# Optimization experiments

Hardware: AMD Instinct MI355X
Metric: run time of the kernel (lower is better)

The kernel has to match this reference:

```python
import jax, jax.numpy as jnp
import numpy as np

N = 100000
E = 1600000
IN_CH = 128
HID = 16
HEADS = 4
OUT_CH = 2
EDGE_DIM = 3
NEG_SLOPE = 0.2


def gat_layer(x, src, dst, e_feat, W, att_src, att_dst, We, att_edge, bias, H, C, concat):
    # x: [N, Fin] -> projected [N, H, C]
    xs = (x @ W).reshape(-1, H, C)
    a_src = jnp.sum(xs * att_src, axis=-1)          # [N, H]
    a_dst = jnp.sum(xs * att_dst, axis=-1)          # [N, H]
    ee = (e_feat @ We).reshape(-1, H, C)            # [E, H, C]
    a_edge = jnp.sum(ee * att_edge, axis=-1)        # [E, H]
    alpha = a_src[src] + a_dst[dst] + a_edge        # [E, H]
    alpha = jax.nn.leaky_relu(alpha, NEG_SLOPE)
    # segment softmax over incoming edges of each dst node
    seg_max = jax.ops.segment_max(alpha, dst, num_segments=N)
    alpha = jnp.exp(alpha - seg_max[dst])
    seg_sum = jax.ops.segment_sum(alpha, dst, num_segments=N)
    alpha = alpha / (seg_sum[dst] + 1e-16)
    # weighted message aggregation
    msg = xs[src] * alpha[:, :, None]               # [E, H, C]
    out = jax.ops.segment_sum(msg, dst, num_segments=N)  # [N, H, C]
    out = out.reshape(-1, H * C) if concat else out.mean(axis=1)
    return out + bias


def setup_inputs() -> dict:
    key = jax.random.key(0)
    ks = jax.random.split(key, 24)
    g = lambda i, shape, scale=0.1: jax.random.normal(ks[i], shape, dtype=jnp.float32) * scale
    inp = {
        "x": jax.random.normal(ks[0], (N, IN_CH), dtype=jnp.float32),
        "edge_index": jax.random.randint(ks[1], (2, E), 0, N, dtype=jnp.int32),
        "edge_feat": jax.random.normal(ks[2], (E, EDGE_DIM), dtype=jnp.float32),
        # edge MLP
        "Em1": g(3, (EDGE_DIM, EDGE_DIM)), "eb1": g(4, (EDGE_DIM,)),
        "Em2": g(5, (EDGE_DIM, EDGE_DIM)), "eb2": g(6, (EDGE_DIM,)),
        # conv1: in -> HID per head, HEADS heads, concat
        "W1": g(7, (IN_CH, HEADS * HID)),
        "as1": g(8, (HEADS, HID)), "ad1": g(9, (HEADS, HID)),
        "We1": g(10, (EDGE_DIM, HEADS * HID)), "ae1": g(11, (HEADS, HID)),
        "b1": g(12, (HEADS * HID,)),
        # conv2: HEADS*HID -> OUT_CH, 1 head, no concat
        "W2": g(13, (HEADS * HID, OUT_CH)),
        "as2": g(14, (1, OUT_CH)), "ad2": g(15, (1, OUT_CH)),
        "We2": g(16, (EDGE_DIM, OUT_CH)), "ae2": g(17, (1, OUT_CH)),
        "b2": g(18, (OUT_CH,)),
    }
    return inp


def reference(x, edge_index, edge_feat,
              Em1, eb1, Em2, eb2,
              W1, as1, ad1, We1, ae1, b1,
              W2, as2, ad2, We2, ae2, b2):
    src, dst = edge_index[0], edge_index[1]
    # edge MLP: Linear -> ReLU -> Linear
    e = jax.nn.relu(edge_feat @ Em1 + eb1) @ Em2 + eb2
    # dropout layers are identity in eval mode
    h = gat_layer(x, src, dst, e, W1, as1, ad1, We1, ae1, b1, HEADS, HID, concat=True)
    h = jax.nn.elu(h)
    out = gat_layer(h, src, dst, e, W2, as2, ad2, We2, ae2, b2, 1, OUT_CH, concat=False)
    return out
```

## Files before the change

### kernel.cpp

```cpp
#include <hip/hip_runtime.h>
#include <hip/hip_fp16.h>
#include <math.h>
#include <stdint.h>

#define NEG_SLOPE 0.2f
#define SCAN_TILE 2048

__device__ __forceinline__ float leaky(float a) { return a > 0.f ? a : NEG_SLOPE * a; }
__device__ __forceinline__ __half2 u2h2(unsigned u) { return *reinterpret_cast<__half2*>(&u); }

__global__ __launch_bounds__(256) void k_pw(const int* __restrict__ dst, int* __restrict__ deg8,
                                            int* __restrict__ pw, int E, int N,
                                            const float* __restrict__ We1, const float* __restrict__ ae1,
                                            const float* __restrict__ We2, const float* __restrict__ ae2,
                                            float* __restrict__ cw) {
    if (blockIdx.x == 0 && threadIdx.x == 0) {
        for (int i = 0; i < 3; i++)
            for (int h = 0; h < 4; h++) {
                float s = 0.f;
                for (int m = 0; m < 16; m++) s += We1[i*64 + h*16 + m] * ae1[h*16 + m];
                cw[i*4 + h] = s;
            }
        for (int i = 0; i < 3; i++) cw[12 + i] = We2[i*2]*ae2[0] + We2[i*2+1]*ae2[1];
    }
    int c = blockIdx.x & 7;
    int* deg = deg8 + (size_t)c * N;
    unsigned ctag = (unsigned)c << 28;
    int base = (blockIdx.x * blockDim.x + threadIdx.x) * 4;
    if (base >= E) return;
    if (base + 3 < E) {
        int4 dv = *reinterpret_cast<const int4*>(&dst[base]);
        int4 pv;
        pv.x = atomicAdd(&deg[dv.x], 1) | ctag;
        pv.y = atomicAdd(&deg[dv.y], 1) | ctag;
        pv.z = atomicAdd(&deg[dv.z], 1) | ctag;
        pv.w = atomicAdd(&deg[dv.w], 1) | ctag;
        *reinterpret_cast<int4*>(&pw[base]) = pv;
    } else {
        for (int i = base; i < E; i++) pw[i] = atomicAdd(&deg[dst[i]], 1) | ctag;
    }
}

__global__ __launch_bounds__(256) void k_scan_partial(const int* __restrict__ deg8, int* __restrict__ tsum, int N) {
    __shared__ int sh[256];
    int b = blockIdx.x, t = threadIdx.x;
    int base = b * SCAN_TILE + t * 8;
    int s = 0;
    if (base + 8 <= N) {
        for (int c = 0; c < 8; c++) {
            const int4* p4 = reinterpret_cast<const int4*>(deg8 + (size_t)c * N + base);
            int4 a = p4[0], bb = p4[1];
            s += a.x + a.y + a.z + a.w + bb.x + bb.y + bb.z + bb.w;
        }
    } else if (base < N) {
        for (int i = base; i < N; i++)
            for (int c = 0; c < 8; c++) s += deg8[(size_t)c * N + i];
    }
    sh[t] = s; __syncthreads();
    for (int o = 128; o > 0; o >>= 1) { if (t < o) sh[t] += sh[t + o]; __syncthreads(); }
    if (t == 0) tsum[b] = sh[0];
}

__global__ void k_scan_tsum(const int* __restrict__ tsum, int* __restrict__ toff,
                            int* __restrict__ rowptr, int nb, int N) {
    if (threadIdx.x == 0 && blockIdx.x == 0) {
        int run = 0;
        for (int i = 0; i < nb; i++) { toff[i] = run; run += tsum[i]; }
        rowptr[N] = run;
    }
}

__global__ __launch_bounds__(256) void k_scan_final(const int* __restrict__ deg8, const int* __restrict__ toff,
        int* __restrict__ rowptr, uint4* __restrict__ slotrec, int N) {
    __shared__ int sh[256];
    int b = blockIdx.x, t = threadIdx.x;
    int base = b * SCAN_TILE + t * 8;
    int vt[8]; int s = 0;
    #pragma unroll
    for (int i = 0; i < 8; i++) {
        int idx = base + i; int tot = 0;
        if (idx < N) {
            #pragma unroll
            for (int c = 0; c < 8; c++) tot += deg8[(size_t)c * N + idx];
        }
        vt[i] = tot; s += tot;
    }
    sh[t] = s; __syncthreads();
    for (int o = 1; o < 256; o <<= 1) {
        int u = (t >= o) ? sh[t - o] : 0;
        __syncthreads();
        sh[t] += u;
        __syncthreads();
    }
    int run = sh[t] - s + toff[b];
    #pragma unroll
    for (int i = 0; i < 8; i++) {
        int idx = base + i;
        if (idx < N) {
            rowptr[idx] = run;
            unsigned lo = 0, hi = 0; int off = 0;
            #pragma unroll
            for (int c = 0; c < 8; c++) {
                unsigned v = (unsigned)off & 0xFFu;
                if (c < 4) lo |= v << (8*c); else hi |= v << (8*(c-4));
                off += deg8[(size_t)c * N + idx];
            }
            slotrec[idx] = make_uint4((unsigned)run, lo, hi, 0u);
            run += vt[i];
        }
    }
}

__global__ __launch_bounds__(256) void k_proj1(const float* __restrict__ x, const float* __restrict__ W1,
        const float* __restrict__ as1, const float* __restrict__ ad1,
        __half* __restrict__ xs1h, float* __restrict__ as1v, float* __restrict__ ad1v, int N) {
    __shared__ float xr[32][128];
    int tid = threadIdx.x;
    int wave = tid >> 6, lane = tid & 63;
    int nbase = blockIdx.x * 32;
    if (nbase + 32 <= N) {
        const float4* x4 = reinterpret_cast<const float4*>(x + (size_t)nbase * 128);
        #pragma unroll
        for (int i = 0; i < 4; i++) {
            int idx = tid + i * 256;
            reinterpret_cast<float4*>(&xr[0][0])[idx] = x4[idx];
        }
    } else {
        for (int i = 0; i < 16; i++) {
            int flat = tid + i * 256;
            int row = flat >> 7, col = flat & 127;
            int n = nbase + row; if (n >= N) n = N - 1;
            xr[row][col] = x[(size_t)n * 128 + col];
        }
    }
    __syncthreads();
    int cc = lane & 15, kk = lane >> 4;
    int nw = wave * 8;
    const float4* W4 = reinterpret_cast<const float4*>(W1);
    float4 acc[8];
    #pragma unroll
    for (int m = 0; m < 8; m++) acc[m] = make_float4(0.f, 0.f, 0.f, 0.f);
    #pragma unroll 4
    for (int k = kk; k < 128; k += 4) {
        float4 wv = W4[k * 16 + cc];
        #pragma unroll
        for (int m = 0; m < 8; m++) {
            float xv = xr[nw + m][k];
            acc[m].x = fmaf(xv, wv.x, acc[m].x);
            acc[m].y = fmaf(xv, wv.y, acc[m].y);
            acc[m].z = fmaf(xv, wv.z, acc[m].z);
            acc[m].w = fmaf(xv, wv.w, acc[m].w);
        }
    }
    float a_s0 = as1[4*cc], a_s1 = as1[4*cc+1], a_s2 = as1[4*cc+2], a_s3 = as1[4*cc+3];
    float a_d0 = ad1[4*cc], a_d1 = ad1[4*cc+1], a_d2 = ad1[4*cc+2], a_d3 = ad1[4*cc+3];
    #pragma unroll
    for (int m = 0; m < 8; m++) {
        float4 a = acc[m];
        a.x += __shfl_xor(a.x, 16, 64); a.y += __shfl_xor(a.y, 16, 64);
        a.z += __shfl_xor(a.z, 16, 64); a.w += __shfl_xor(a.w, 16, 64);
        a.x += __shfl_xor(a.x, 32, 64); a.y += __shfl_xor(a.y, 32, 64);
        a.z += __shfl_xor(a.z, 32, 64); a.w += __shfl_xor(a.w, 32, 64);
        float ps = a.x*a_s0 + a.y*a_s1 + a.z*a_s2 + a.w*a_s3;
        float pd = a.x*a_d0 + a.y*a_d1 + a.z*a_d2 + a.w*a_d3;
        ps += __shfl_xor(ps, 1, 64); ps += __shfl_xor(ps, 2, 64);
        pd += __shfl_xor(pd, 1, 64); pd += __shfl_xor(pd, 2, 64);
        if (kk == 0) {
            int n = nbase + nw + m; if (n >= N) n = N - 1;
            __half2 h01 = __halves2half2(__float2half_rn(a.x), __float2half_rn(a.y));
            __half2 h23 = __halves2half2(__float2half_rn(a.z), __float2half_rn(a.w));
            uint2 st;
            st.x = *reinterpret_cast<unsigned*>(&h01);
            st.y = *reinterpret_cast<unsigned*>(&h23);
            *reinterpret_cast<uint2*>(&xs1h[(size_t)n*64 + 4*cc]) = st;
            if ((cc & 3) == 0) {
                int h = cc >> 2;
                as1v[n*4 + h] = ps;
                ad1v[n*4 + h] = pd;
            }
        }
    }
}

__global__ __launch_bounds__(256) void k_payload(const float* __restrict__ ef,
                       const float* __restrict__ Em1, const float* __restrict__ eb1,
                       const float* __restrict__ Em2, const float* __restrict__ eb2,
                       const float* __restrict__ cw,
                       const int* __restrict__ src, const int* __restrict__ dst,
                       const int* __restrict__ pw,
                       const float4* __restrict__ as1v4,
                       const uint4* __restrict__ slotrec,
                       uint4* __restrict__ csr_pk, int E) {
    int base = (blockIdx.x * blockDim.x + threadIdx.x) * 4;
    if (base >= E) return;
    int cnt = min(4, E - base);

    float f[4][3]; int sv[4], dv[4], pv[4];
    if (cnt == 4) {
        const float4* ef4 = reinterpret_cast<const float4*>(ef);
        float4 a = ef4[base*3/4 + 0], b = ef4[base*3/4 + 1], c = ef4[base*3/4 + 2];
        f[0][0]=a.x; f[0][1]=a.y; f[0][2]=a.z;
        f[1][0]=a.w; f[1][1]=b.x; f[1][2]=b.y;
        f[2][0]=b.z; f[2][1]=b.w; f[2][2]=c.x;
        f[3][0]=c.y; f[3][1]=c.z; f[3][2]=c.w;
        int4 s4 = *reinterpret_cast<const int4*>(&src[base]);
        int4 d4 = *reinterpret_cast<const int4*>(&dst[base]);
        int4 p4 = *reinterpret_cast<const int4*>(&pw[base]);
        sv[0]=s4.x; sv[1]=s4.y; sv[2]=s4.z; sv[3]=s4.w;
        dv[0]=d4.x; dv[1]=d4.y; dv[2]=d4.z; dv[3]=d4.w;
        pv[0]=p4.x; pv[1]=p4.y; pv[2]=p4.z; pv[3]=p4.w;
    } else {
        for (int i = 0; i < cnt; i++) {
            f[i][0]=ef[(base+i)*3+0]; f[i][1]=ef[(base+i)*3+1]; f[i][2]=ef[(base+i)*3+2];
            sv[i]=src[base+i]; dv[i]=dst[base+i]; pv[i]=pw[base+i];
        }
    }

    #pragma unroll
    for (int i = 0; i < 4; i++) {
        if (i >= cnt) break;
        float f0=f[i][0], f1=f[i][1], f2=f[i][2];
        float t0 = fmaxf(f0*Em1[0]+f1*Em1[3]+f2*Em1[6]+eb1[0], 0.f);
        float t1 = fmaxf(f0*Em1[1]+f1*Em1[4]+f2*Em1[7]+eb1[1], 0.f);
        float t2 = fmaxf(f0*Em1[2]+f1*Em1[5]+f2*Em1[8]+eb1[2], 0.f);
        float u0 = t0*Em2[0]+t1*Em2[3]+t2*Em2[6]+eb2[0];
        float u1 = t0*Em2[1]+t1*Em2[4]+t2*Em2[7]+eb2[1];
        float u2 = t0*Em2[2]+t1*Em2[5]+t2*Em2[8]+eb2[2];
        int s = sv[i], d = dv[i];
        float4 av = as1v4[s];
        uint4  r  = slotrec[d];
        int c  = ((unsigned)pv[i]) >> 28;
        int ps = pv[i] & 0x0FFFFFFF;
        unsigned pre = ((c < 4) ? (r.y >> (8*c)) : (r.z >> (8*(c-4)))) & 0xFFu;
        int slot = (int)r.x + (int)pre + ps;
        float b0 = av.x + u0*cw[0] + u1*cw[4] + u2*cw[8];
        float b1 = av.y + u0*cw[1] + u1*cw[5] + u2*cw[9];
        float b2 = av.z + u0*cw[2] + u1*cw[6] + u2*cw[10];
        float b3 = av.w + u0*cw[3] + u1*cw[7] + u2*cw[11];
        float e2 = u0*cw[12] + u1*cw[13] + u2*cw[14];
        __half2 lo = __halves2half2(__float2half_rn(b0), __float2half_rn(b1));
        __half2 hi = __halves2half2(__float2half_rn(b2), __float2half_rn(b3));
        uint4 pki;
        pki.x = (unsigned)s;
        pki.y = *reinterpret_cast<unsigned*>(&lo);
        pki.z = *reinterpret_cast<unsigned*>(&hi);
        pki.w = *reinterpret_cast<unsigned*>(&e2);
        csr_pk[slot] = pki;
    }
}

__global__ __launch_bounds__(256, 4) void k_gat1(
        const int* __restrict__ rowptr, const uint4* __restrict__ csr_pk,
        const __half* __restrict__ xs1h, const float4* __restrict__ ad1v4,
        const float* __restrict__ b1, const float* __restrict__ W2,
        const float* __restrict__ as2, const float* __restrict__ ad2,
        float2* __restrict__ pk2, float* __restrict__ ad2v, int N) {
    int wave = threadIdx.x >> 6, lane = threadIdx.x & 63;
    int d = blockIdx.x * 4 + wave;
    if (d >= N) return;
    int beg = rowptr[d], end = rowptr[d+1];
    float4 ad4 = ad1v4[d];
    int cg = lane & 15, e4 = lane >> 4;
    int hh = cg >> 2;
    const __half* xbase = xs1h + 4 * cg;
    float4 acc = make_float4(0.f, 0.f, 0.f, 0.f);
    float4 wv  = make_float4(0.f, 0.f, 0.f, 0.f);
    for (int off = beg; off < end; off += 16) {
        int j = off + cg;
        bool valid = j < end;
        uint4 p = valid ? csr_pk[j] : make_uint4(0u, 0u, 0u, 0u);
        int si = (int)p.x;
        float w0 = 0.f, w1 = 0.f, w2 = 0.f, w3 = 0.f;
        if (valid) {
            __half2 l01 = u2h2(p.y), l23 = u2h2(p.z);
            w0 = __expf(leaky(__low2float(l01)  + ad4.x));
            w1 = __expf(leaky(__high2float(l01) + ad4.y));
            w2 = __expf(leaky(__low2float(l23)  + ad4.z));
            w3 = __expf(leaky(__high2float(l23) + ad4.w));
        }
        wv.x += w0; wv.y += w1; wv.z += w2; wv.w += w3;
        __half2 wy2 = __halves2half2(__float2half_rn(w0), __float2half_rn(w1));
        __half2 wz2 = __halves2half2(__float2half_rn(w2), __float2half_rn(w3));
        unsigned wy = *reinterpret_cast<unsigned*>(&wy2);
        unsigned wz = *reinterpret_cast<unsigned*>(&wz2);
        int st0, st1, st2, st3; float wt0, wt1, wt2, wt3;
        {
            int sl0 = 0*4 + e4, sl1 = 1*4 + e4, sl2 = 2*4 + e4, sl3 = 3*4 + e4;
            st0 = __shfl(si, sl0, 16); st1 = __shfl(si, sl1, 16);
            st2 = __shfl(si, sl2, 16); st3 = __shfl(si, sl3, 16);
            unsigned y0 = __shfl(wy, sl0, 16), z0 = __shfl(wz, sl0, 16);
            unsigned y1 = __shfl(wy, sl1, 16), z1 = __shfl(wz, sl1, 16);
            unsigned y2 = __shfl(wy, sl2, 16), z2 = __shfl(wz, sl2, 16);
            unsigned y3 = __shfl(wy, sl3, 16), z3 = __shfl(wz, sl3, 16);
            unsigned q0 = (hh < 2) ? y0 : z0;
            unsigned q1 = (hh < 2) ? y1 : z1;
            unsigned q2 = (hh < 2) ? y2 : z2;
            unsigned q3 = (hh < 2) ? y3 : z3;
            wt0 = (hh & 1) ? __high2float(u2h2(q0)) : __low2float(u2h2(q0));
            wt1 = (hh & 1) ? __high2float(u2h2(q1)) : __low2float(u2h2(q1));
            wt2 = (hh & 1) ? __high2float(u2h2(q2)) : __low2float(u2h2(q2));
            wt3 = (hh & 1) ? __high2float(u2h2(q3)) : __low2float(u2h2(q3));
        }
        uint2 g0 = *reinterpret_cast<const uint2*>(xbase + ((size_t)st0 << 6));
        uint2 g1 = *reinterpret_cast<const uint2*>(xbase + ((size_t)st1 << 6));
        uint2 g2 = *reinterpret_cast<const uint2*>(xbase + ((size_t)st2 << 6));
        uint2 g3 = *reinterpret_cast<const uint2*>(xbase + ((size_t)st3 << 6));
        __half2 a, b;
        a = u2h2(g0.x); b = u2h2(g0.y);
        acc.x = fmaf(wt0, __low2float(a), acc.x); acc.y = fmaf(wt0, __high2float(a), acc.y);
        acc.z = fmaf(wt0, __low2float(b), acc.z); acc.w = fmaf(wt0, __high2float(b), acc.w);
        a = u2h2(g1.x); b = u2h2(g1.y);
        acc.x = fmaf(wt1, __low2float(a), acc.x); acc.y = fmaf(wt1, __high2float(a), acc.y);
        acc.z = fmaf(wt1, __low2float(b), acc.z); acc.w = fmaf(wt1, __high2float(b), acc.w);
        a = u2h2(g2.x); b = u2h2(g2.y);
        acc.x = fmaf(wt2, __low2float(a), acc.x); acc.y = fmaf(wt2, __high2float(a), acc.y);
        acc.z = fmaf(wt2, __low2float(b), acc.z); acc.w = fmaf(wt2, __high2float(b), acc.w);
        a = u2h2(g3.x); b = u2h2(g3.y);
        acc.x = fmaf(wt3, __low2float(a), acc.x); acc.y = fmaf(wt3, __high2float(a), acc.y);
        acc.z = fmaf(wt3, __low2float(b), acc.z); acc.w = fmaf(wt3, __high2float(b), acc.w);
    }
    acc.x += __shfl_xor(acc.x, 16, 64); acc.y += __shfl_xor(acc.y, 16, 64);
    acc.z += __shfl_xor(acc.z, 16, 64); acc.w += __shfl_xor(acc.w, 16, 64);
    acc.x += __shfl_xor(acc.x, 32, 64); acc.y += __shfl_xor(acc.y, 32, 64);
    acc.z += __shfl_xor(acc.z, 32, 64); acc.w += __shfl_xor(acc.w, 32, 64);
    #pragma unroll
    for (int o = 1; o <= 8; o <<= 1) {
        wv.x += __shfl_xor(wv.x, o, 16); wv.y += __shfl_xor(wv.y, o, 16);
        wv.z += __shfl_xor(wv.z, o, 16); wv.w += __shfl_xor(wv.w, o, 16);
    }
    float sm = (hh == 0) ? wv.x : (hh == 1) ? wv.y : (hh == 2) ? wv.z : wv.w;
    float inv = 1.f / (sm + 1e-16f);
    float v0 = acc.x * inv + b1[4*cg + 0];
    float v1 = acc.y * inv + b1[4*cg + 1];
    float v2 = acc.z * inv + b1[4*cg + 2];
    float v3 = acc.w * inv + b1[4*cg + 3];
    v0 = v0 > 0.f ? v0 : expm1f(v0);
    v1 = v1 > 0.f ? v1 : expm1f(v1);
    v2 = v2 > 0.f ? v2 : expm1f(v2);
    v3 = v3 > 0.f ? v3 : expm1f(v3);
    float p0 = v0*W2[(4*cg+0)*2] + v1*W2[(4*cg+1)*2] + v2*W2[(4*cg+2)*2] + v3*W2[(4*cg+3)*2];
    float p1 = v0*W2[(4*cg+0)*2+1] + v1*W2[(4*cg+1)*2+1] + v2*W2[(4*cg+2)*2+1] + v3*W2[(4*cg+3)*2+1];
    #pragma unroll
    for (int o = 1; o <= 8; o <<= 1) { p0 += __shfl_xor(p0, o, 16); p1 += __shfl_xor(p1, o, 16); }
    if (lane == 0) {
        float2 q;
        q.x = p0*as2[0] + p1*as2[1];
        __half2 xv = __halves2half2(__float2half_rn(p0), __float2half_rn(p1));
        q.y = *reinterpret_cast<float*>(&xv);
        pk2[d] = q;
        ad2v[d] = p0*ad2[0] + p1*ad2[1];
    }
}

__global__ __launch_bounds__(256) void k_gat2(
        const int* __restrict__ rowptr, const uint4* __restrict__ csr_pk,
        const float2* __restrict__ pk2, const float* __restrict__ ad2v,
        const float* __restrict__ b2, float* __restrict__ out, int N) {
    int t = blockIdx.x * blockDim.x + threadIdx.x;
    int d = t >> 4, j16 = t & 15;
    if (d >= N) return;
    int beg = rowptr[d], end = rowptr[d+1];
    float add = ad2v[d];
    float sm = 0.f, p0 = 0.f, p1 = 0.f;
    for (int off = beg; off < end; off += 16) {
        int j = off + j16;
        if (j < end) {
            uint4 p = csr_pk[j];
            int s = (int)p.x;
            float ea2 = *reinterpret_cast<float*>(&p.w);
            float2 q = pk2[s];
            float w = __expf(leaky(q.x + add + ea2));
            __half2 xv = *reinterpret_cast<__half2*>(&q.y);
            p0 = fmaf(w, __low2float(xv), p0);
            p1 = fmaf(w, __high2float(xv), p1);
            sm += w;
        }
    }
    #pragma unroll
    for (int o = 1; o < 16; o <<= 1) {
        sm += __shfl_xor(sm, o, 16);
        p0 += __shfl_xor(p0, o, 16);
        p1 += __shfl_xor(p1, o, 16);
    }
    if (j16 == 0) {
        float inv = 1.f / (sm + 1e-16f);
        out[d*2+0] = p0*inv + b2[0];
        out[d*2+1] = p1*inv + b2[1];
    }
}

extern "C" void kernel_launch(void* const* d_in, const int* in_sizes, int n_in,
                              void* d_out, int out_size, void* d_ws, size_t ws_size,
                              hipStream_t stream) {
    const float* x   = (const float*)d_in[0];
    const int*   ei  = (const int*)d_in[1];
    const float* ef  = (const float*)d_in[2];
    const float* Em1 = (const float*)d_in[3];
    const float* eb1 = (const float*)d_in[4];
    const float* Em2 = (const float*)d_in[5];
    const float* eb2 = (const float*)d_in[6];
    const float* W1  = (const float*)d_in[7];
    const float* as1 = (const float*)d_in[8];
    const float* ad1 = (const float*)d_in[9];
    const float* We1 = (const float*)d_in[10];
    const float* ae1 = (const float*)d_in[11];
    const float* b1  = (const float*)d_in[12];
    const float* W2  = (const float*)d_in[13];
    const float* as2 = (const float*)d_in[14];
    const float* ad2 = (const float*)d_in[15];
    const float* We2 = (const float*)d_in[16];
    const float* ae2 = (const float*)d_in[17];
    const float* b2  = (const float*)d_in[18];

    const int N = in_sizes[0] / 128;
    const int E = in_sizes[1] / 2;
    const int* srcp = ei;
    const int* dstp = ei + E;

    uintptr_t w = (uintptr_t)d_ws;
    auto alloc = [&](size_t bytes) -> void* {
        uintptr_t p = w; w += (bytes + 255) & ~(size_t)255; return (void*)p;
    };
    const int nb = (N + SCAN_TILE - 1) / SCAN_TILE;
    int*    deg8    = (int*)alloc((size_t)8 * N * sizeof(int));
    int*    rowptr  = (int*)alloc(((size_t)N + 1) * sizeof(int));
    int*    tsum    = (int*)alloc((size_t)nb * sizeof(int));
    int*    toff    = (int*)alloc((size_t)(nb + 1) * sizeof(int));
    float*  cw      = (float*)alloc(16 * sizeof(float));
    int*    pw      = (int*)alloc((size_t)E * sizeof(int));
    uint4*  slotrec = (uint4*)alloc((size_t)N * sizeof(uint4));
    uint4*  csr_pk  = (uint4*)alloc((size_t)E * sizeof(uint4));
    __half* xs1h    = (__half*)alloc((size_t)N * 64 * sizeof(__half));
    float*  as1v    = (float*)alloc((size_t)N * 4 * sizeof(float));
    float*  ad1v    = (float*)alloc((size_t)N * 4 * sizeof(float));
    float2* pk2     = (float2*)alloc((size_t)N * sizeof(float2));
    float*  ad2v    = (float*)alloc((size_t)N * sizeof(float));

    const int B = 256;

    hipMemsetAsync(deg8, 0, (size_t)8 * N * sizeof(int), stream);
    k_pw<<<(E/4+B-1)/B + 1, B, 0, stream>>>(dstp, deg8, pw, E, N, We1, ae1, We2, ae2, cw);
    k_scan_partial<<<nb, 256, 0, stream>>>(deg8, tsum, N);
    k_scan_tsum<<<1, 64, 0, stream>>>(tsum, toff, rowptr, nb, N);
    k_scan_final<<<nb, 256, 0, stream>>>(deg8, toff, rowptr, slotrec, N);
    k_proj1<<<(N+31)/32, 256, 0, stream>>>(x, W1, as1, ad1, xs1h, as1v, ad1v, N);
    k_payload<<<(E/4+B-1)/B + 1, B, 0, stream>>>(ef, Em1, eb1, Em2, eb2, cw,
                                                 srcp, dstp, pw, (const float4*)as1v,
                                                 slotrec, csr_pk, E);
    k_gat1<<<(N+3)/4, 256, 0, stream>>>(rowptr, csr_pk, xs1h, (const float4*)ad1v,
                                        b1, W2, as2, ad2, pk2, ad2v, N);
    k_gat2<<<(N*16+B-1)/B, B, 0, stream>>>(rowptr, csr_pk, pk2, ad2v, b2, (float*)d_out, N);
}
```

Measured before the change: 254.1 us.

## Remap GAT1 wave lanes to head-major layout to cut exp and shuffle work

Reassigns the 64 lanes in the layer-1 aggregation kernel so each 16-lane group owns one head. Each lane now computes one exp per edge instead of four, and broadcasts float weights directly, dropping the half packing and select logic. The reductions at the end are rewritten to match the new lane map. In exchange, each gather now reads 16 contiguous halves per head rather than spreading one source row across the wave, which may change memory coalescing.

```diff
diff --git a/kernel.cpp b/kernel.cpp
--- a/kernel.cpp
+++ b/kernel.cpp
@@ -260,47 +260,35 @@
     if (d >= N) return;
     int beg = rowptr[d], end = rowptr[d+1];
     float4 ad4 = ad1v4[d];
-    int cg = lane & 15, e4 = lane >> 4;
-    int hh = cg >> 2;
-    const __half* xbase = xs1h + 4 * cg;
+    int sub = lane & 15;
+    int hh  = lane >> 4;
+    int e4  = (lane >> 2) & 3;
+    int cq  = lane & 3;
+    float adh = (hh == 0) ? ad4.x : (hh == 1) ? ad4.y : (hh == 2) ? ad4.z : ad4.w;
+    const __half* xbase = xs1h + (hh * 16 + cq * 4);
     float4 acc = make_float4(0.f, 0.f, 0.f, 0.f);
-    float4 wv  = make_float4(0.f, 0.f, 0.f, 0.f);
+    float wsum = 0.f;
     for (int off = beg; off < end; off += 16) {
-        int j = off + cg;
+        int j = off + sub;
         bool valid = j < end;
         uint4 p = valid ? csr_pk[j] : make_uint4(0u, 0u, 0u, 0u);
         int si = (int)p.x;
-        float w0 = 0.f, w1 = 0.f, w2 = 0.f, w3 = 0.f;
+        float w = 0.f;
         if (valid) {
-            __half2 l01 = u2h2(p.y), l23 = u2h2(p.z);
-            w0 = __expf(leaky(__low2float(l01)  + ad4.x));
-            w1 = __expf(leaky(__high2float(l01) + ad4.y));
-            w2 = __expf(leaky(__low2float(l23)  + ad4.z));
-            w3 = __expf(leaky(__high2float(l23) + ad4.w));
-        }
-        wv.x += w0; wv.y += w1; wv.z += w2; wv.w += w3;
-        __half2 wy2 = __halves2half2(__float2half_rn(w0), __float2half_rn(w1));
-        __half2 wz2 = __halves2half2(__float2half_rn(w2), __float2half_rn(w3));
-        unsigned wy = *reinterpret_cast<unsigned*>(&wy2);
-        unsigned wz = *reinterpret_cast<unsigned*>(&wz2);
-        int st0, st1, st2, st3; float wt0, wt1, wt2, wt3;
-        {
-            int sl0 = 0*4 + e4, sl1 = 1*4 + e4, sl2 = 2*4 + e4, sl3 = 3*4 + e4;
-            st0 = __shfl(si, sl0, 16); st1 = __shfl(si, sl1, 16);
-            st2 = __shfl(si, sl2, 16); st3 = __shfl(si, sl3, 16);
-            unsigned y0 = __shfl(wy, sl0, 16), z0 = __shfl(wz, sl0, 16);
-            unsigned y1 = __shfl(wy, sl1, 16), z1 = __shfl(wz, sl1, 16);
-            unsigned y2 = __shfl(wy, sl2, 16), z2 = __shfl(wz, sl2, 16);
-            unsigned y3 = __shfl(wy, sl3, 16), z3 = __shfl(wz, sl3, 16);
-            unsigned q0 = (hh < 2) ? y0 : z0;
-            unsigned q1 = (hh < 2) ? y1 : z1;
-            unsigned q2 = (hh < 2) ? y2 : z2;
-            unsigned q3 = (hh < 2) ? y3 : z3;
-            wt0 = (hh & 1) ? __high2float(u2h2(q0)) : __low2float(u2h2(q0));
-            wt1 = (hh & 1) ? __high2float(u2h2(q1)) : __low2float(u2h2(q1));
-            wt2 = (hh & 1) ? __high2float(u2h2(q2)) : __low2float(u2h2(q2));
-            wt3 = (hh & 1) ? __high2float(u2h2(q3)) : __low2float(u2h2(q3));
-        }
+            unsigned lw = (hh < 2) ? p.y : p.z;
+            __half2 lh = u2h2(lw);
+            float lg = (hh & 1) ? __high2float(lh) : __low2float(lh);
+            w = __expf(leaky(lg + adh));
+        }
+        wsum += w;
+        int st0 = __shfl(si, e4 + 0, 16);
+        int st1 = __shfl(si, e4 + 4, 16);
+        int st2 = __shfl(si, e4 + 8, 16);
+        int st3 = __shfl(si, e4 + 12, 16);
+        float wt0 = __shfl(w, e4 + 0, 16);
+        float wt1 = __shfl(w, e4 + 4, 16);
+        float wt2 = __shfl(w, e4 + 8, 16);
+        float wt3 = __shfl(w, e4 + 12, 16);
         uint2 g0 = *reinterpret_cast<const uint2*>(xbase + ((size_t)st0 << 6));
         uint2 g1 = *reinterpret_cast<const uint2*>(xbase + ((size_t)st1 << 6));
         uint2 g2 = *reinterpret_cast<const uint2*>(xbase + ((size_t)st2 << 6));
@@ -319,29 +307,33 @@
         acc.x = fmaf(wt3, __low2float(a), acc.x); acc.y = fmaf(wt3, __high2float(a), acc.y);
         acc.z = fmaf(wt3, __low2float(b), acc.z); acc.w = fmaf(wt3, __high2float(b), acc.w);
     }
-    acc.x += __shfl_xor(acc.x, 16, 64); acc.y += __shfl_xor(acc.y, 16, 64);
-    acc.z += __shfl_xor(acc.z, 16, 64); acc.w += __shfl_xor(acc.w, 16, 64);
-    acc.x += __shfl_xor(acc.x, 32, 64); acc.y += __shfl_xor(acc.y, 32, 64);
-    acc.z += __shfl_xor(acc.z, 32, 64); acc.w += __shfl_xor(acc.w, 32, 64);
-    #pragma unroll
-    for (int o = 1; o <= 8; o <<= 1) {
-        wv.x += __shfl_xor(wv.x, o, 16); wv.y += __shfl_xor(wv.y, o, 16);
-        wv.z += __shfl_xor(wv.z, o, 16); wv.w += __shfl_xor(wv.w, o, 16);
-    }
-    float sm = (hh == 0) ? wv.x : (hh == 1) ? wv.y : (hh == 2) ? wv.z : wv.w;
-    float inv = 1.f / (sm + 1e-16f);
-    float v0 = acc.x * inv + b1[4*cg + 0];
-    float v1 = acc.y * inv + b1[4*cg + 1];
-    float v2 = acc.z * inv + b1[4*cg + 2];
-    float v3 = acc.w * inv + b1[4*cg + 3];
-    v0 = v0 > 0.f ? v0 : expm1f(v0);
-    v1 = v1 > 0.f ? v1 : expm1f(v1);
-    v2 = v2 > 0.f ? v2 : expm1f(v2);
-    v3 = v3 > 0.f ? v3 : expm1f(v3);
-    float p0 = v0*W2[(4*cg+0)*2] + v1*W2[(4*cg+1)*2] + v2*W2[(4*cg+2)*2] + v3*W2[(4*cg+3)*2];
-    float p1 = v0*W2[(4*cg+0)*2+1] + v1*W2[(4*cg+1)*2+1] + v2*W2[(4*cg+2)*2+1] + v3*W2[(4*cg+3)*2+1];
-    #pragma unroll
-    for (int o = 1; o <= 8; o <<= 1) { p0 += __shfl_xor(p0, o, 16); p1 += __shfl_xor(p1, o, 16); }
+    acc.x += __shfl_xor(acc.x, 4, 64); acc.y += __shfl_xor(acc.y, 4, 64);
+    acc.z += __shfl_xor(acc.z, 4, 64); acc.w += __shfl_xor(acc.w, 4, 64);
+    acc.x += __shfl_xor(acc.x, 8, 64); acc.y += __shfl_xor(acc.y, 8, 64);
+    acc.z += __shfl_xor(acc.z, 8, 64); acc.w += __shfl_xor(acc.w, 8, 64);
+    wsum += __shfl_xor(wsum, 1, 64);
+    wsum += __shfl_xor(wsum, 2, 64);
+    wsum += __shfl_xor(wsum, 4, 64);
+    wsum += __shfl_xor(wsum, 8, 64);
+    float inv = 1.f / (wsum + 1e-16f);
+    float p0 = 0.f, p1 = 0.f;
+    if (e4 == 0) {
+        int cb = hh * 16 + cq * 4;
+        float v0 = acc.x * inv + b1[cb + 0];
+        float v1 = acc.y * inv + b1[cb + 1];
+        float v2 = acc.z * inv + b1[cb + 2];
+        float v3 = acc.w * inv + b1[cb + 3];
+        v0 = v0 > 0.f ? v0 : expm1f(v0);
+        v1 = v1 > 0.f ? v1 : expm1f(v1);
+        v2 = v2 > 0.f ? v2 : expm1f(v2);
+        v3 = v3 > 0.f ? v3 : expm1f(v3);
+        p0 = v0*W2[(cb+0)*2]   + v1*W2[(cb+1)*2]   + v2*W2[(cb+2)*2]   + v3*W2[(cb+3)*2];
+        p1 = v0*W2[(cb+0)*2+1] + v1*W2[(cb+1)*2+1] + v2*W2[(cb+2)*2+1] + v3*W2[(cb+3)*2+1];
+    }
+    p0 += __shfl_xor(p0, 1, 64);  p1 += __shfl_xor(p1, 1, 64);
+    p0 += __shfl_xor(p0, 2, 64);  p1 += __shfl_xor(p1, 2, 64);
+    p0 += __shfl_xor(p0, 16, 64); p1 += __shfl_xor(p1, 16, 64);
+    p0 += __shfl_xor(p0, 32, 64); p1 += __shfl_xor(p1, 32, 64);
     if (lane == 0) {
         float2 q;
         q.x = p0*as2[0] + p1*as2[1];
```

Result: no change. 254.1 us (+0.0%).
